# Optimization experiments

Hardware: AMD Instinct MI355X
Metric: run time of the kernel (lower is better)

## Reference

```python
import jax, jax.numpy as jnp
import numpy as np

N, D = 262144, 512
EPS = 1e-6  # flax LayerNorm default


def setup_inputs() -> dict:
    key = jax.random.key(0)
    kx, kw = jax.random.split(key)
    x = jax.random.normal(kx, (N, D), dtype=jnp.float32)
    # LayerNorm params (flax defaults: scale init ones, bias init zeros)
    ln_scale = jnp.ones((D,), dtype=jnp.float32)
    ln_bias = jnp.zeros((D,), dtype=jnp.float32)
    # Dense params (lecun_normal kernel init approximated by scaled normal)
    kernel = jax.random.normal(kw, (D, D), dtype=jnp.float32) / jnp.sqrt(jnp.float32(D))
    bias = jnp.zeros((D,), dtype=jnp.float32)
    return {"x": x, "ln_scale": ln_scale, "ln_bias": ln_bias, "kernel": kernel, "bias": bias}


def reference(x, ln_scale, ln_bias, kernel, bias):
    # LayerNorm over last axis
    mu = jnp.mean(x, axis=-1, keepdims=True)
    var = jnp.mean(jnp.square(x - mu), axis=-1, keepdims=True)
    out = (x - mu) * jax.lax.rsqrt(var + EPS) * ln_scale + ln_bias
    # activation -> Dense -> residual add
    h = jax.nn.relu(out)
    return x + jnp.dot(h, kernel) + bias
```

## Files before the change

kernel.cpp:

```cpp
#include <hip/hip_runtime.h>
#include <hip/hip_bf16.h>

#define DD 512
#define BM 64
#define THREADS 1024

typedef __attribute__((ext_vector_type(8))) short short8;
typedef __attribute__((ext_vector_type(4))) float f32x4;

__device__ __forceinline__ unsigned short f2bf(float f) {
  union { float f; unsigned u; } v; v.f = f;
  unsigned r = v.u + 0x7FFFu + ((v.u >> 16) & 1u);
  return (unsigned short)(r >> 16);
}
__device__ __forceinline__ float bf2f(unsigned short u) {
  union { unsigned u; float f; } v; v.u = ((unsigned)u) << 16;
  return v.f;
}

__global__ void prep_bpack(const float* __restrict__ W, unsigned short* __restrict__ Bpack) {
  const int tid = blockIdx.x * blockDim.x + threadIdx.x;
  const int n = tid & 511, k = tid >> 9;
  const float w = W[(size_t)k * DD + n];
  const int nb = n >> 4, lo = n & 15;
  const int kt = k >> 5, hi = (k >> 3) & 3, j = k & 7;
  const int lane = hi * 16 + lo;
  Bpack[(((size_t)(nb * 16 + kt)) * 64 + lane) * 8 + j] = f2bf(w);
}

__global__ __launch_bounds__(THREADS, 4)
void fused_ln_gemm(const float* __restrict__ x, const float* __restrict__ lns,
                   const float* __restrict__ lnb, const unsigned short* __restrict__ Bpack,
                   const float* __restrict__ bias, float* __restrict__ out) {
  __shared__ unsigned short Alds[BM * 512];
  __shared__ unsigned short Xlds[BM * 512];

  const int t = threadIdx.x;
  const int lane = t & 63, lo = lane & 15, hi = lane >> 4;
  const int w = t >> 6;
  const long row0 = (long)blockIdx.x * BM;

  {
    const int r = t >> 4, g = t & 15;
    const float* xr = x + (row0 + r) * DD + g * 4;
    float4 v[8];
    float s = 0.f, s2 = 0.f;
    #pragma unroll
    for (int i = 0; i < 8; ++i) {
      v[i] = *(const float4*)(xr + i * 64);
      s  += (v[i].x + v[i].y) + (v[i].z + v[i].w);
      s2 += v[i].x * v[i].x + v[i].y * v[i].y + v[i].z * v[i].z + v[i].w * v[i].w;
    }
    #pragma unroll
    for (int m = 1; m < 16; m <<= 1) {
      s  += __shfl_xor(s,  m, 64);
      s2 += __shfl_xor(s2, m, 64);
    }
    const float mu   = s * (1.f / 512.f);
    const float var  = fmaxf(s2 * (1.f / 512.f) - mu * mu, 0.f);
    const float rstd = rsqrtf(var + 1e-6f);
    #pragma unroll
    for (int i = 0; i < 8; ++i) {
      const int c = g * 4 + i * 64;
      const float4 sc = *(const float4*)(lns + c);
      const float4 bi = *(const float4*)(lnb + c);
      ushort4 hu;
      hu.x = f2bf(fmaxf((v[i].x - mu) * rstd * sc.x + bi.x, 0.f));
      hu.y = f2bf(fmaxf((v[i].y - mu) * rstd * sc.y + bi.y, 0.f));
      hu.z = f2bf(fmaxf((v[i].z - mu) * rstd * sc.z + bi.z, 0.f));
      hu.w = f2bf(fmaxf((v[i].w - mu) * rstd * sc.w + bi.w, 0.f));
      ushort4 xu = { f2bf(v[i].x), f2bf(v[i].y), f2bf(v[i].z), f2bf(v[i].w) };
      const unsigned a = (unsigned)(r * 1024 + g * 8 + i * 128) ^ (unsigned)((r & 7) << 4);
      *(ushort4*)((char*)Alds + a) = hu;
      *(ushort4*)((char*)Xlds + a) = xu;
    }
  }
  __syncthreads();

  unsigned abase[4];
  #pragma unroll
  for (int m = 0; m < 4; ++m)
    abase[m] = (unsigned)((m * 16 + lo) * 1024 + hi * 16);
  const unsigned asw = (unsigned)((lo & 7) << 4);

  const short8* bbase = (const short8*)Bpack + (size_t)(w * 2) * 1024 + lane;

  short8 rb[3][2];
#define LOADB(s, kt)                                                          \
  { rb[s][0] = bbase[(0 * 16 + (kt)) * 64];                                   \
    rb[s][1] = bbase[(1 * 16 + (kt)) * 64]; }

  LOADB(0, 0);
  LOADB(1, 1);
  __builtin_amdgcn_sched_barrier(0);

  f32x4 acc[4][2] = {};

  #pragma unroll
  for (int kt = 0; kt < 16; ++kt) {
    const int cur = kt % 3;
    if (kt + 2 < 16) {
      const int nxt = (kt + 2) % 3;
      LOADB(nxt, kt + 2);
    }
    __builtin_amdgcn_sched_barrier(0);
    short8 a[4];
    #pragma unroll
    for (int m = 0; m < 4; ++m)
      a[m] = *(const short8*)((const char*)Alds + ((abase[m] + (unsigned)kt * 64) ^ asw));
    #pragma unroll
    for (int m = 0; m < 4; ++m) {
      acc[m][0] = __builtin_amdgcn_mfma_f32_16x16x32_bf16(a[m], rb[cur][0], acc[m][0], 0, 0, 0);
      acc[m][1] = __builtin_amdgcn_mfma_f32_16x16x32_bf16(a[m], rb[cur][1], acc[m][1], 0, 0, 0);
    }
  }
#undef LOADB

  const int col0 = w * 32 + lo;
  const float bv0 = bias[col0];
  const float bv1 = bias[col0 + 16];
  #pragma unroll
  for (int m = 0; m < 4; ++m) {
    #pragma unroll
    for (int q = 0; q < 4; ++q) {
      const int rl = m * 16 + hi * 4 + q;
      const unsigned xb = (unsigned)(rl * 1024 + col0 * 2) ^ (unsigned)((rl & 7) << 4);
      const float xv0 = bf2f(*(const unsigned short*)((const char*)Xlds + xb));
      const float xv1 = bf2f(*(const unsigned short*)((const char*)Xlds + (xb ^ 32u)));
      float* o = out + (row0 + rl) * DD + col0;
      o[0]  = acc[m][0][q] + xv0 + bv0;
      o[16] = acc[m][1][q] + xv1 + bv1;
    }
  }
}

extern "C" void kernel_launch(void* const* d_in, const int* in_sizes, int n_in,
                              void* d_out, int out_size, void* d_ws, size_t ws_size,
                              hipStream_t stream) {
  const float* x    = (const float*)d_in[0];
  const float* lns  = (const float*)d_in[1];
  const float* lnb  = (const float*)d_in[2];
  const float* W    = (const float*)d_in[3];
  const float* bias = (const float*)d_in[4];
  float* out = (float*)d_out;
  unsigned short* Bpack = (unsigned short*)d_ws;

  const int nrows = in_sizes[0] / DD;

  prep_bpack<<<DD * DD / 256, 256, 0, stream>>>(W, Bpack);
  fused_ln_gemm<<<nrows / BM, THREADS, 0, stream>>>(x, lns, lnb, Bpack, bias, out);
}
```

Baseline: 295.4 us.

## Make fused LN-GEMM persistent over 16 row tiles with next-tile x prefetch

Each block now handles 16 consecutive 64-row tiles instead of one, issuing the global loads of the next tile's x rows into registers before running the current tile's MFMA loop. LayerNorm and LDS staging for the next tile happen after the epilogue, separated by raw s_barrier plus lgkmcnt waits. The goal is to hide HBM load latency behind compute and amortise block launch and setup. In exchange the grid shrinks to 256 blocks of 1024 threads, roughly one per CU, which may leave little occupancy to cover the serialized LN phase. The B double buffer is cut from 3 to 2 stages.

```diff
diff --git a/kernel.cpp b/kernel.cpp
--- a/kernel.cpp
+++ b/kernel.cpp
@@ -3,6 +3,7 @@
 
 #define DD 512
 #define BM 64
+#define TILES 16
 #define THREADS 1024
 
 typedef __attribute__((ext_vector_type(8))) short short8;
@@ -38,16 +39,26 @@
   const int t = threadIdx.x;
   const int lane = t & 63, lo = lane & 15, hi = lane >> 4;
   const int w = t >> 6;
-  const long row0 = (long)blockIdx.x * BM;
+  const int r = t >> 4, g = t & 15;
+  const long base = (long)blockIdx.x * (BM * TILES);
 
-  {
-    const int r = t >> 4, g = t & 15;
-    const float* xr = x + (row0 + r) * DD + g * 4;
-    float4 v[8];
+  const int col0 = w * 32 + lo;
+  const float bv0 = bias[col0];
+  const float bv1 = bias[col0 + 16];
+
+  unsigned abase[4];
+  #pragma unroll
+  for (int m = 0; m < 4; ++m)
+    abase[m] = (unsigned)((m * 16 + lo) * 1024 + hi * 16);
+  const unsigned asw = (unsigned)((lo & 7) << 4);
+  const short8* bbase = (const short8*)Bpack + (size_t)(w * 2) * 1024 + lane;
+
+  float4 v[8];
+
+  auto ln_store = [&]() {
     float s = 0.f, s2 = 0.f;
     #pragma unroll
     for (int i = 0; i < 8; ++i) {
-      v[i] = *(const float4*)(xr + i * 64);
       s  += (v[i].x + v[i].y) + (v[i].z + v[i].w);
       s2 += v[i].x * v[i].x + v[i].y * v[i].y + v[i].z * v[i].z + v[i].w * v[i].w;
     }
@@ -74,63 +85,71 @@
       *(ushort4*)((char*)Alds + a) = hu;
       *(ushort4*)((char*)Xlds + a) = xu;
     }
+  };
+
+  {
+    const float* xr = x + (base + r) * DD + g * 4;
+    #pragma unroll
+    for (int i = 0; i < 8; ++i) v[i] = *(const float4*)(xr + i * 64);
   }
-  __syncthreads();
+  ln_store();
+  asm volatile("s_waitcnt lgkmcnt(0)" ::: "memory");
+  __builtin_amdgcn_s_barrier();
 
-  unsigned abase[4];
-  #pragma unroll
-  for (int m = 0; m < 4; ++m)
-    abase[m] = (unsigned)((m * 16 + lo) * 1024 + hi * 16);
-  const unsigned asw = (unsigned)((lo & 7) << 4);
+  #pragma unroll 1
+  for (int it = 0; it < TILES; ++it) {
+    const long trow0 = base + (long)it * BM;
 
-  const short8* bbase = (const short8*)Bpack + (size_t)(w * 2) * 1024 + lane;
+    if (it + 1 < TILES) {
+      const float* xr2 = x + (trow0 + BM + r) * DD + g * 4;
+      #pragma unroll
+      for (int i = 0; i < 8; ++i) v[i] = *(const float4*)(xr2 + i * 64);
+    }
 
-  short8 rb[3][2];
-#define LOADB(s, kt)                                                          \
-  { rb[s][0] = bbase[(0 * 16 + (kt)) * 64];                                   \
-    rb[s][1] = bbase[(1 * 16 + (kt)) * 64]; }
+    f32x4 acc[4][2] = {};
+    short8 rb[2][2];
+#define LOADB(s_, kt)                                                        \
+    { rb[s_][0] = bbase[(0 * 16 + (kt)) * 64];                               \
+      rb[s_][1] = bbase[(1 * 16 + (kt)) * 64]; }
 
-  LOADB(0, 0);
-  LOADB(1, 1);
-  __builtin_amdgcn_sched_barrier(0);
-
-  f32x4 acc[4][2] = {};
-
-  #pragma unroll
-  for (int kt = 0; kt < 16; ++kt) {
-    const int cur = kt % 3;
-    if (kt + 2 < 16) {
-      const int nxt = (kt + 2) % 3;
-      LOADB(nxt, kt + 2);
+    LOADB(0, 0);
+    __builtin_amdgcn_sched_barrier(0);
+    #pragma unroll
+    for (int kt = 0; kt < 16; ++kt) {
+      if (kt + 1 < 16) LOADB((kt + 1) & 1, kt + 1);
+      __builtin_amdgcn_sched_barrier(0);
+      #pragma unroll
+      for (int m = 0; m < 4; ++m) {
+        const short8 a = *(const short8*)((const char*)Alds + ((abase[m] + (unsigned)kt * 64) ^ asw));
+        acc[m][0] = __builtin_amdgcn_mfma_f32_16x16x32_bf16(a, rb[kt & 1][0], acc[m][0], 0, 0, 0);
+        acc[m][1] = __builtin_amdgcn_mfma_f32_16x16x32_bf16(a, rb[kt & 1][1], acc[m][1], 0, 0, 0);
+      }
     }
-    __builtin_amdgcn_sched_barrier(0);
-    short8 a[4];
-    #pragma unroll
-    for (int m = 0; m < 4; ++m)
-      a[m] = *(const short8*)((const char*)Alds + ((abase[m] + (unsigned)kt * 64) ^ asw));
-    #pragma unroll
-    for (int m = 0; m < 4; ++m) {
-      acc[m][0] = __builtin_amdgcn_mfma_f32_16x16x32_bf16(a[m], rb[cur][0], acc[m][0], 0, 0, 0);
-      acc[m][1] = __builtin_amdgcn_mfma_f32_16x16x32_bf16(a[m], rb[cur][1], acc[m][1], 0, 0, 0);
-    }
-  }
 #undef LOADB
 
-  const int col0 = w * 32 + lo;
-  const float bv0 = bias[col0];
-  const float bv1 = bias[col0 + 16];
-  #pragma unroll
-  for (int m = 0; m < 4; ++m) {
-    #pragma unroll
-    for (int q = 0; q < 4; ++q) {
-      const int rl = m * 16 + hi * 4 + q;
-      const unsigned xb = (unsigned)(rl * 1024 + col0 * 2) ^ (unsigned)((rl & 7) << 4);
-      const float xv0 = bf2f(*(const unsigned short*)((const char*)Xlds + xb));
-      const float xv1 = bf2f(*(const unsigned short*)((const char*)Xlds + (xb ^ 32u)));
-      float* o = out + (row0 + rl) * DD + col0;
-      o[0]  = acc[m][0][q] + xv0 + bv0;
-      o[16] = acc[m][1][q] + xv1 + bv1;
+    {
+      float* oc = out + (trow0 + hi * 4) * DD + col0;
+      #pragma unroll
+      for (int m = 0; m < 4; ++m) {
+        #pragma unroll
+        for (int q = 0; q < 4; ++q) {
+          const int rl = m * 16 + hi * 4 + q;
+          const unsigned xb = (unsigned)(rl * 1024 + col0 * 2) ^ (unsigned)((rl & 7) << 4);
+          const float xv0 = bf2f(*(const unsigned short*)((const char*)Xlds + xb));
+          const float xv1 = bf2f(*(const unsigned short*)((const char*)Xlds + (xb ^ 32u)));
+          float* o = oc + (m * 16 + q) * DD;
+          o[0]  = acc[m][0][q] + xv0 + bv0;
+          o[16] = acc[m][1][q] + xv1 + bv1;
+        }
+      }
     }
+
+    __builtin_amdgcn_s_barrier();
+
+    if (it + 1 < TILES) ln_store();
+
+    asm volatile("s_waitcnt lgkmcnt(0)" ::: "memory");
+    __builtin_amdgcn_s_barrier();
   }
 }
 
@@ -148,5 +167,5 @@
   const int nrows = in_sizes[0] / DD;
 
   prep_bpack<<<DD * DD / 256, 256, 0, stream>>>(W, Bpack);
-  fused_ln_gemm<<<nrows / BM, THREADS, 0, stream>>>(x, lns, lnb, Bpack, bias, out);
+  fused_ln_gemm<<<nrows / (BM * TILES), THREADS, 0, stream>>>(x, lns, lnb, Bpack, bias, out);
 }
```

Result: slower. 1.079 ms (+265.3%).
